# Optimization experiments

Hardware: AMD Instinct MI355X
Metric: run time of the kernel (lower is better)

The kernel has to match this reference:

```python
import jax, jax.numpy as jnp
import numpy as np

EPS_REG = 0.1     # Sinkhorn regularization eps (init arg)
MAX_ITER = 50     # max Sinkhorn iterations (init arg)
THRESH = 0.1      # early-stop threshold from the torch code

N, P1, P2, D = 4, 2048, 2048, 64


def setup_inputs() -> dict:
    key = jax.random.key(0)
    k1, k2, k3 = jax.random.split(key, 3)
    x = jax.random.normal(k1, (N, P1, D), dtype=jnp.float32)
    y = jax.random.normal(k2, (N, P2, D), dtype=jnp.float32)
    M = jax.random.normal(k3, (D, D), dtype=jnp.float32)
    return {"x": x, "y": y, "M": M}


def _cost_matrix(x, y, M):
    # C_ij = (x_i - y_j) M (x_i - y_j)^T, expanded to avoid the [N,P1,P2,D]
    # difference tensor the torch code materializes (identical math):
    #   C = x M x^T (diag) + y M y^T (diag) - x M y^T - (y M x^T)^T
    xM = jnp.einsum('npd,de->npe', x, M)
    yM = jnp.einsum('nqd,de->nqe', y, M)
    dx = jnp.einsum('npd,npd->np', xM, x)  # [N,P1]
    dy = jnp.einsum('nqd,nqd->nq', yM, y)  # [N,P2]
    cross = jnp.einsum('npd,nqd->npq', xM, y) + jnp.einsum('nqd,npd->npq', yM, x)
    return dx[:, :, None] + dy[:, None, :] - cross  # [N,P1,P2]


def _bias(C, u, v, eps):
    # M_ij = (-C_ij + u_i + v_j) / eps
    return (-C + u[..., :, None] + v[..., None, :]) / eps


def _sinkhorn(C, eps):
    n, p1, p2 = C.shape
    log_mu = jnp.log(jnp.full((n, p1), 1.0 / p1, C.dtype) + 1e-8)
    log_nu = jnp.log(jnp.full((n, p2), 1.0 / p2, C.dtype) + 1e-8)
    u0 = jnp.zeros((n, p1), C.dtype)
    v0 = jnp.zeros((n, p2), C.dtype)

    def step(carry, _):
        u, v, active = carry
        u1 = u
        u_new = eps * (log_mu - jax.scipy.special.logsumexp(_bias(C, u, v, eps), axis=-1)) + u
        u = jnp.where(active, u_new, u)
        v_new = eps * (log_nu - jax.scipy.special.logsumexp(_bias(C, u, v, eps), axis=-2)) + v
        v = jnp.where(active, v_new, v)
        err = jnp.mean(jnp.sum(jnp.abs(u - u1), axis=-1))
        active = active & (err >= THRESH)  # freeze updates once converged (== torch break)
        return (u, v, active), None

    (u, v, _), _ = jax.lax.scan(step, (u0, v0, jnp.asarray(True)), None, length=MAX_ITER)
    return u, v


def reference(x, y, M):
    eps = EPS_REG
    C = _cost_matrix(x, y, M)
    u, v = _sinkhorn(C, eps)
    pi = jnp.exp(_bias(C, u, v, eps))
    cost = jnp.sum(pi * C, axis=(-2, -1))  # reduction='none' -> shape [N]
    return cost, pi, C
```

## Files before the change

kernel.cpp:

```cpp
#include <hip/hip_runtime.h>
#include <cstdint>
#include <cstddef>

#define NB 4
#define P1 2048
#define P2 2048
#define DD 64
#define ITER 50
#define EPS 0.1f
#define INV_EPS 10.0f
#define THRESH 0.1f
#define LOG_MU -7.6245985f
#define ELOG (-0.76245985f)
#define MU_VAL 0.00048829125f
#define ERRSLOTS 32
#define RP (P2 / 4)
#define PCHUNKS 128

__global__ void prep0(const float* __restrict__ M, float* __restrict__ S,
                      float* __restrict__ errAcc, int* __restrict__ active,
                      float* __restrict__ cost) {
    int t = threadIdx.x;
    for (int k = t; k < DD * DD; k += 256) {
        int d = k >> 6, e = k & 63;
        S[k] = M[d * DD + e] + M[e * DD + d];
    }
    for (int k = t; k < ITER * ERRSLOTS; k += 256) errAcc[k] = 0.0f;
    if (t < 64) active[t] = (t == 0) ? 1 : 0;
    if (t < NB) cost[t] = 0.0f;
}

__global__ __launch_bounds__(256) void prep1(const float* __restrict__ x,
                                             const float* __restrict__ y,
                                             const float* __restrict__ S,
                                             float* __restrict__ xS,
                                             float* __restrict__ dx,
                                             float* __restrict__ dy,
                                             float* __restrict__ u,
                                             float* __restrict__ v) {
    __shared__ float Sl[DD * DD];
    int t = threadIdx.x;
    for (int k = t; k < DD * DD; k += 256) Sl[k] = S[k];
    __syncthreads();
    int wave = t >> 6, lane = t & 63;
    int r = blockIdx.x * 4 + wave;
    bool isX = r < NB * P1;
    const float* src = isX ? x : y;
    int rr = isX ? r : r - NB * P1;
    float xv = src[(size_t)rr * DD + lane];
    float acc = 0.0f;
    #pragma unroll
    for (int d = 0; d < DD; ++d) {
        float xd = __shfl(xv, d, 64);
        acc = fmaf(xd, Sl[d * DD + lane], acc);
    }
    float p = acc * xv;
    #pragma unroll
    for (int o = 32; o; o >>= 1) p += __shfl_xor(p, o, 64);
    if (isX) {
        xS[(size_t)rr * DD + lane] = acc;
        if (lane == 0) { dx[rr] = 0.5f * p; u[rr] = 0.0f; }
    } else {
        if (lane == 0) { dy[rr] = 0.5f * p; v[rr] = 0.0f; }
    }
}

__global__ __launch_bounds__(256) void gemmC(const float* __restrict__ xS,
                                             const float* __restrict__ y,
                                             const float* __restrict__ dx,
                                             const float* __restrict__ dy,
                                             float* __restrict__ C) {
    __shared__ float xs[64][68];
    __shared__ float ys[64][68];
    int n = blockIdx.z;
    int i0 = blockIdx.y * 64, j0 = blockIdx.x * 64;
    int t = threadIdx.x;

    #pragma unroll
    for (int k = 0; k < 4; ++k) {
        int f = t + 256 * k;
        int row = f >> 4;
        int c4 = f & 15;
        float4 a = ((const float4*)xS)[((size_t)(n * P1 + i0 + row)) * (DD / 4) + c4];
        xs[4 * c4 + 0][row] = a.x; xs[4 * c4 + 1][row] = a.y;
        xs[4 * c4 + 2][row] = a.z; xs[4 * c4 + 3][row] = a.w;
        float4 b = ((const float4*)y)[((size_t)(n * P2 + j0 + row)) * (DD / 4) + c4];
        ys[4 * c4 + 0][row] = b.x; ys[4 * c4 + 1][row] = b.y;
        ys[4 * c4 + 2][row] = b.z; ys[4 * c4 + 3][row] = b.w;
    }
    __syncthreads();

    int tx = t & 15, ty = t >> 4;
    float acc[4][4] = {};
    #pragma unroll
    for (int e = 0; e < 64; ++e) {
        float4 a = *(const float4*)&xs[e][4 * ty];
        float4 b = *(const float4*)&ys[e][4 * tx];
        acc[0][0] = fmaf(a.x, b.x, acc[0][0]); acc[0][1] = fmaf(a.x, b.y, acc[0][1]);
        acc[0][2] = fmaf(a.x, b.z, acc[0][2]); acc[0][3] = fmaf(a.x, b.w, acc[0][3]);
        acc[1][0] = fmaf(a.y, b.x, acc[1][0]); acc[1][1] = fmaf(a.y, b.y, acc[1][1]);
        acc[1][2] = fmaf(a.y, b.z, acc[1][2]); acc[1][3] = fmaf(a.y, b.w, acc[1][3]);
        acc[2][0] = fmaf(a.z, b.x, acc[2][0]); acc[2][1] = fmaf(a.z, b.y, acc[2][1]);
        acc[2][2] = fmaf(a.z, b.z, acc[2][2]); acc[2][3] = fmaf(a.z, b.w, acc[2][3]);
        acc[3][0] = fmaf(a.w, b.x, acc[3][0]); acc[3][1] = fmaf(a.w, b.y, acc[3][1]);
        acc[3][2] = fmaf(a.w, b.z, acc[3][2]); acc[3][3] = fmaf(a.w, b.w, acc[3][3]);
    }

    int iBase = i0 + ty * 4, jBase = j0 + tx * 4;
    float4 dy4 = *(const float4*)&dy[n * P2 + jBase];
    #pragma unroll
    for (int r = 0; r < 4; ++r) {
        float dxv = dx[n * P1 + iBase + r];
        float4 o;
        o.x = dxv + dy4.x - acc[r][0];
        o.y = dxv + dy4.y - acc[r][1];
        o.z = dxv + dy4.z - acc[r][2];
        o.w = dxv + dy4.w - acc[r][3];
        *(float4*)&C[((size_t)(n * P1 + iBase + r)) * P2 + jBase] = o;
    }
}

__device__ __forceinline__ void load_row8(float4 dst[8], const float4* base, int lane) {
    #pragma unroll
    for (int k = 0; k < 8; ++k) dst[k] = base[lane + 64 * k];
}

__device__ __forceinline__ float row_lse(float4 c[8], float ai, const float* bl, int lane) {
    float m = -3.4e38f;
    #pragma unroll
    for (int k = 0; k < 8; ++k) {
        float4 vv = ((const float4*)bl)[lane + 64 * k];
        c[k].x = (ai - c[k].x) + vv.x;
        c[k].y = (ai - c[k].y) + vv.y;
        c[k].z = (ai - c[k].z) + vv.z;
        c[k].w = (ai - c[k].w) + vv.w;
        m = fmaxf(m, fmaxf(fmaxf(c[k].x, c[k].y), fmaxf(c[k].z, c[k].w)));
    }
    #pragma unroll
    for (int o = 1; o < 64; o <<= 1) m = fmaxf(m, __shfl_xor(m, o, 64));
    float s = 0.0f;
    #pragma unroll
    for (int k = 0; k < 8; ++k)
        s += __expf((c[k].x - m) * INV_EPS) + __expf((c[k].y - m) * INV_EPS) +
             __expf((c[k].z - m) * INV_EPS) + __expf((c[k].w - m) * INV_EPS);
    #pragma unroll
    for (int o = 1; o < 64; o <<= 1) s += __shfl_xor(s, o, 64);
    return EPS * __logf(s) + m;
}

__device__ __forceinline__ void mergec(float& m, float& s, float q) {
    float nm = fmaxf(m, q);
    s = s * __expf((m - nm) * INV_EPS) + __expf((q - nm) * INV_EPS);
    m = nm;
}
__device__ __forceinline__ void mergems(float& m, float& s, float mo, float so) {
    float nm = fmaxf(m, mo);
    s = s * __expf((m - nm) * INV_EPS) + so * __expf((mo - nm) * INV_EPS);
    m = nm;
}
__device__ __forceinline__ void merge44(float4& m, float4& s, float4 mo, float4 so) {
    mergems(m.x, s.x, mo.x, so.x);
    mergems(m.y, s.y, mo.y, so.y);
    mergems(m.z, s.z, mo.z, so.z);
    mergems(m.w, s.w, mo.w, so.w);
}

__device__ __forceinline__ void merge_row(float4 M[8], float4 S[8],
                                          const float4 q[8], float dr) {
    #pragma unroll
    for (int k = 0; k < 8; ++k) {
        mergec(M[k].x, S[k].x, q[k].x + dr);
        mergec(M[k].y, S[k].y, q[k].y + dr);
        mergec(M[k].z, S[k].z, q[k].z + dr);
        mergec(M[k].w, S[k].w, q[k].w + dr);
    }
}

__global__ __launch_bounds__(256) void iter_pass(const float* __restrict__ C,
                                                 float* __restrict__ u,
                                                 const float* __restrict__ v,
                                                 float* __restrict__ pm,
                                                 float* __restrict__ ps,
                                                 float* __restrict__ errAcc,
                                                 const int* __restrict__ active,
                                                 int t_iter) {
    if (!active[t_iter]) return;
    __shared__ float bl[P2];
    __shared__ float4 LM[4][512];
    __shared__ float4 LS[4][512];
    __shared__ float da_s[4];
    int t = threadIdx.x;
    int n = blockIdx.x >> 7;
    int i0 = (blockIdx.x & (PCHUNKS - 1)) * 16;
    {
        const float4* bsrc = (const float4*)(v + n * P2);
        ((float4*)bl)[t] = bsrc[t];
        ((float4*)bl)[t + 256] = bsrc[t + 256];
    }
    __syncthreads();

    int wave = t >> 6, lane = t & 63;
    int irow = i0 + wave * 4;
    float* arow = u + n * P1 + irow;
    float a0 = arow[0], a1 = arow[1], a2 = arow[2], a3 = arow[3];
    const float4* base = (const float4*)(C + ((size_t)(n * P1 + irow)) * P2);

    float4 M[8], S[8];
    #pragma unroll
    for (int k = 0; k < 8; ++k) {
        M[k] = make_float4(-3.4e38f, -3.4e38f, -3.4e38f, -3.4e38f);
        S[k] = make_float4(0.0f, 0.0f, 0.0f, 0.0f);
    }

    float4 A[8], B[8];
    load_row8(A, base, lane);
    load_row8(B, base + RP, lane);
    float l0 = row_lse(A, a0, bl, lane);
    float d0 = ELOG - l0;
    merge_row(M, S, A, d0);
    load_row8(A, base + 2 * RP, lane);
    float l1 = row_lse(B, a1, bl, lane);
    float d1 = ELOG - l1;
    merge_row(M, S, B, d1);
    load_row8(B, base + 3 * RP, lane);
    float l2 = row_lse(A, a2, bl, lane);
    float d2 = ELOG - l2;
    merge_row(M, S, A, d2);
    float l3 = row_lse(B, a3, bl, lane);
    float d3 = ELOG - l3;
    merge_row(M, S, B, d3);

    if (lane == 0) {
        arow[0] = a0 + d0; arow[1] = a1 + d1;
        arow[2] = a2 + d2; arow[3] = a3 + d3;
        da_s[wave] = fabsf(d0) + fabsf(d1) + fabsf(d2) + fabsf(d3);
    }

    #pragma unroll
    for (int k = 0; k < 8; ++k) {
        LM[wave][lane + 64 * k] = M[k];
        LS[wave][lane + 64 * k] = S[k];
    }
    __syncthreads();

    float4* pm4 = (float4*)pm;
    float4* ps4 = (float4*)ps;
    size_t pb4 = (size_t)blockIdx.x * 512;
    #pragma unroll
    for (int sl = 0; sl < 2; ++sl) {
        int slot = t + 256 * sl;
        float4 m = LM[0][slot], s = LS[0][slot];
        merge44(m, s, LM[1][slot], LS[1][slot]);
        merge44(m, s, LM[2][slot], LS[2][slot]);
        merge44(m, s, LM[3][slot], LS[3][slot]);
        pm4[pb4 + slot] = m;
        ps4[pb4 + slot] = s;
    }

    if (t == 0) {
        atomicAdd(&errAcc[t_iter * ERRSLOTS + (blockIdx.x & (ERRSLOTS - 1))],
                  da_s[0] + da_s[1] + da_s[2] + da_s[3]);
    }
}

__global__ __launch_bounds__(256) void v_comb(const float* __restrict__ pm,
                                              const float* __restrict__ ps,
                                              float* __restrict__ v,
                                              const float* __restrict__ errAcc,
                                              int* __restrict__ active,
                                              int t_iter) {
    if (blockIdx.x == 0 && threadIdx.x == 0) {
        float e = 0.0f;
        #pragma unroll
        for (int q = 0; q < ERRSLOTS; ++q) e += errAcc[t_iter * ERRSLOTS + q];
        if (active[t_iter] && (e * 0.25f >= THRESH)) active[t_iter + 1] = 1;
    }
    if (!active[t_iter]) return;
    __shared__ float LMv[4][64];
    __shared__ float LSv[4][64];
    int t = threadIdx.x, wave = t >> 6, lane = t & 63;
    int n = blockIdx.x >> 5;
    int j = ((blockIdx.x & 31) << 6) + lane;
    const float* pmb = pm + ((size_t)(n * PCHUNKS + wave * 32)) * P2 + j;
    const float* psb = ps + ((size_t)(n * PCHUNKS + wave * 32)) * P2 + j;
    float m0 = -3.4e38f, s0 = 0.0f, m1 = -3.4e38f, s1 = 0.0f;
    float m2 = -3.4e38f, s2 = 0.0f, m3 = -3.4e38f, s3 = 0.0f;
    #pragma unroll
    for (int c = 0; c < 32; c += 4) {
        mergems(m0, s0, pmb[(size_t)(c + 0) * P2], psb[(size_t)(c + 0) * P2]);
        mergems(m1, s1, pmb[(size_t)(c + 1) * P2], psb[(size_t)(c + 1) * P2]);
        mergems(m2, s2, pmb[(size_t)(c + 2) * P2], psb[(size_t)(c + 2) * P2]);
        mergems(m3, s3, pmb[(size_t)(c + 3) * P2], psb[(size_t)(c + 3) * P2]);
    }
    mergems(m0, s0, m1, s1);
    mergems(m2, s2, m3, s3);
    mergems(m0, s0, m2, s2);
    LMv[wave][lane] = m0; LSv[wave][lane] = s0;
    __syncthreads();
    if (wave == 0) {
        float m = LMv[0][lane], s = LSv[0][lane];
        mergems(m, s, LMv[1][lane], LSv[1][lane]);
        mergems(m, s, LMv[2][lane], LSv[2][lane]);
        mergems(m, s, LMv[3][lane], LSv[3][lane]);
        float lse = EPS * __logf(s) + m;
        v[n * P2 + j] = v[n * P2 + j] + ELOG - lse;
    }
}

__device__ __forceinline__ float row_sum(float4 c[8], float aiv, const float* bl,
                                         int lane) {
    float s = 0.0f;
    #pragma unroll
    for (int k = 0; k < 8; ++k) {
        float4 vv = ((const float4*)bl)[lane + 64 * k];
        c[k].x = __expf(fmaf(c[k].x, -INV_EPS, aiv + vv.x));
        c[k].y = __expf(fmaf(c[k].y, -INV_EPS, aiv + vv.y));
        c[k].z = __expf(fmaf(c[k].z, -INV_EPS, aiv + vv.z));
        c[k].w = __expf(fmaf(c[k].w, -INV_EPS, aiv + vv.w));
        s += (c[k].x + c[k].y) + (c[k].z + c[k].w);
    }
    #pragma unroll
    for (int o = 1; o < 64; o <<= 1) s += __shfl_xor(s, o, 64);
    return s;
}

__device__ __forceinline__ void acc_row(float4 S[8], const float4 q[8], float ed) {
    #pragma unroll
    for (int k = 0; k < 8; ++k) {
        S[k].x = fmaf(q[k].x, ed, S[k].x);
        S[k].y = fmaf(q[k].y, ed, S[k].y);
        S[k].z = fmaf(q[k].z, ed, S[k].z);
        S[k].w = fmaf(q[k].w, ed, S[k].w);
    }
}

__global__ __launch_bounds__(256) void iter_fast(const float* __restrict__ C,
                                                 float* __restrict__ u,
                                                 const float* __restrict__ v,
                                                 float* __restrict__ ps,
                                                 float* __restrict__ errAcc,
                                                 const int* __restrict__ active,
                                                 int t_iter) {
    if (!active[t_iter]) return;
    __shared__ float bl[P2];
    __shared__ float4 LS[4][512];
    __shared__ float da_s[4];
    int t = threadIdx.x;
    int n = blockIdx.x >> 7;
    int i0 = (blockIdx.x & (PCHUNKS - 1)) * 16;
    {
        const float4* bsrc = (const float4*)(v + n * P2);
        float4 b0 = bsrc[t], b1 = bsrc[t + 256];
        b0.x *= INV_EPS; b0.y *= INV_EPS; b0.z *= INV_EPS; b0.w *= INV_EPS;
        b1.x *= INV_EPS; b1.y *= INV_EPS; b1.z *= INV_EPS; b1.w *= INV_EPS;
        ((float4*)bl)[t] = b0;
        ((float4*)bl)[t + 256] = b1;
    }
    __syncthreads();

    int wave = t >> 6, lane = t & 63;
    int irow = i0 + wave * 4;
    float* arow = u + n * P1 + irow;
    float a0 = arow[0], a1 = arow[1], a2 = arow[2], a3 = arow[3];
    const float4* base = (const float4*)(C + ((size_t)(n * P1 + irow)) * P2);

    float4 S[8];
    #pragma unroll
    for (int k = 0; k < 8; ++k) S[k] = make_float4(0.0f, 0.0f, 0.0f, 0.0f);

    float4 X[8], Y[8], Z[8];
    load_row8(X, base, lane);
    load_row8(Y, base + RP, lane);
    load_row8(Z, base + 2 * RP, lane);
    float s0 = row_sum(X, a0 * INV_EPS, bl, lane);
    float d0 = ELOG - EPS * __logf(s0);
    acc_row(S, X, __fdividef(MU_VAL, s0));
    load_row8(X, base + 3 * RP, lane);
    float s1 = row_sum(Y, a1 * INV_EPS, bl, lane);
    float d1 = ELOG - EPS * __logf(s1);
    acc_row(S, Y, __fdividef(MU_VAL, s1));
    float s2 = row_sum(Z, a2 * INV_EPS, bl, lane);
    float d2 = ELOG - EPS * __logf(s2);
    acc_row(S, Z, __fdividef(MU_VAL, s2));
    float s3 = row_sum(X, a3 * INV_EPS, bl, lane);
    float d3 = ELOG - EPS * __logf(s3);
    acc_row(S, X, __fdividef(MU_VAL, s3));

    if (lane == 0) {
        arow[0] = a0 + d0; arow[1] = a1 + d1;
        arow[2] = a2 + d2; arow[3] = a3 + d3;
        da_s[wave] = fabsf(d0) + fabsf(d1) + fabsf(d2) + fabsf(d3);
    }

    #pragma unroll
    for (int k = 0; k < 8; ++k) LS[wave][lane + 64 * k] = S[k];
    __syncthreads();

    float4* ps4 = (float4*)ps;
    size_t pb4 = (size_t)blockIdx.x * 512;
    #pragma unroll
    for (int sl = 0; sl < 2; ++sl) {
        int slot = t + 256 * sl;
        float4 x0 = LS[0][slot], x1 = LS[1][slot];
        float4 x2 = LS[2][slot], x3 = LS[3][slot];
        float4 o;
        o.x = (x0.x + x1.x) + (x2.x + x3.x);
        o.y = (x0.y + x1.y) + (x2.y + x3.y);
        o.z = (x0.z + x1.z) + (x2.z + x3.z);
        o.w = (x0.w + x1.w) + (x2.w + x3.w);
        ps4[pb4 + slot] = o;
    }

    if (t == 0) {
        atomicAdd(&errAcc[t_iter * ERRSLOTS + (blockIdx.x & (ERRSLOTS - 1))],
                  da_s[0] + da_s[1] + da_s[2] + da_s[3]);
    }
}

__global__ __launch_bounds__(256) void v_fast(const float* __restrict__ ps,
                                              float* __restrict__ v,
                                              const float* __restrict__ errAcc,
                                              int* __restrict__ active,
                                              int t_iter) {
    if (blockIdx.x == 0 && threadIdx.x == 0) {
        float e = 0.0f;
        #pragma unroll
        for (int q = 0; q < ERRSLOTS; ++q) e += errAcc[t_iter * ERRSLOTS + q];
        if (active[t_iter] && (e * 0.25f >= THRESH)) active[t_iter + 1] = 1;
    }
    if (!active[t_iter]) return;
    __shared__ float LSv[4][64];
    int t = threadIdx.x, wave = t >> 6, lane = t & 63;
    int n = blockIdx.x >> 5;
    int j = ((blockIdx.x & 31) << 6) + lane;
    const float* psb = ps + ((size_t)(n * PCHUNKS + wave * 32)) * P2 + j;
    float s0 = 0.0f, s1 = 0.0f, s2 = 0.0f, s3 = 0.0f;
    #pragma unroll
    for (int c = 0; c < 32; c += 4) {
        s0 += psb[(size_t)(c + 0) * P2];
        s1 += psb[(size_t)(c + 1) * P2];
        s2 += psb[(size_t)(c + 2) * P2];
        s3 += psb[(size_t)(c + 3) * P2];
    }
    LSv[wave][lane] = (s0 + s1) + (s2 + s3);
    __syncthreads();
    if (wave == 0) {
        float s = (LSv[0][lane] + LSv[1][lane]) + (LSv[2][lane] + LSv[3][lane]);
        v[n * P2 + j] = v[n * P2 + j] + ELOG - EPS * __logf(s);
    }
}

__device__ __forceinline__ float row_pi(const float4 c[8], float ui, const float* vl,
                                        int lane, float4* prow) {
    float acc = 0.0f;
    #pragma unroll
    for (int k = 0; k < 8; ++k) {
        float4 vv = ((const float4*)vl)[lane + 64 * k];
        float4 p;
        p.x = __expf(((ui - c[k].x) + vv.x) * INV_EPS);
        p.y = __expf(((ui - c[k].y) + vv.y) * INV_EPS);
        p.z = __expf(((ui - c[k].z) + vv.z) * INV_EPS);
        p.w = __expf(((ui - c[k].w) + vv.w) * INV_EPS);
        prow[lane + 64 * k] = p;
        acc += p.x * c[k].x + p.y * c[k].y + p.z * c[k].z + p.w * c[k].w;
    }
    return acc;
}

__global__ __launch_bounds__(256) void final_pass(const float* __restrict__ C,
                                                  const float* __restrict__ u,
                                                  const float* __restrict__ v,
                                                  float* __restrict__ pi,
                                                  float* __restrict__ cost) {
    __shared__ float vl[P2];
    __shared__ float red[4];
    int t = threadIdx.x;
    int n = blockIdx.x >> 7;
    int i0 = (blockIdx.x & 127) * 16;
    {
        const float4* vsrc = (const float4*)(v + n * P2);
        ((float4*)vl)[t] = vsrc[t];
        ((float4*)vl)[t + 256] = vsrc[t + 256];
    }
    __syncthreads();

    int wave = t >> 6, lane = t & 63;
    int irow = i0 + wave * 4;
    const float* urow = u + n * P1 + irow;
    float u0 = urow[0], u1 = urow[1], u2 = urow[2], u3 = urow[3];
    const float4* base = (const float4*)(C + ((size_t)(n * P1 + irow)) * P2);
    float4* pbase = (float4*)(pi + ((size_t)(n * P1 + irow)) * P2);

    float4 A[8], B[8];
    load_row8(A, base, lane);
    load_row8(B, base + RP, lane);
    float acc = row_pi(A, u0, vl, lane, pbase);
    load_row8(A, base + 2 * RP, lane);
    acc += row_pi(B, u1, vl, lane, pbase + RP);
    load_row8(B, base + 3 * RP, lane);
    acc += row_pi(A, u2, vl, lane, pbase + 2 * RP);
    acc += row_pi(B, u3, vl, lane, pbase + 3 * RP);

    #pragma unroll
    for (int o = 1; o < 64; o <<= 1) acc += __shfl_xor(acc, o, 64);
    if (lane == 0) red[wave] = acc;
    __syncthreads();
    if (t == 0) atomicAdd(&cost[n], red[0] + red[1] + red[2] + red[3]);
}

extern "C" void kernel_launch(void* const* d_in, const int* in_sizes, int n_in,
                              void* d_out, int out_size, void* d_ws, size_t ws_size,
                              hipStream_t stream) {
    const float* x = (const float*)d_in[0];
    const float* y = (const float*)d_in[1];
    const float* M = (const float*)d_in[2];
    float* out = (float*)d_out;
    float* cost = out;
    float* pi = out + NB;
    float* C = out + NB + (size_t)NB * P1 * P2;

    float* ws = (float*)d_ws;
    float* S      = ws;
    float* xS     = S + DD * DD;
    float* dx     = xS + (size_t)NB * P1 * DD;
    float* dy     = dx + NB * P1;
    float* u      = dy + NB * P2;
    float* v      = u + NB * P1;
    float* errAcc = v + NB * P2;
    int*   active = (int*)(errAcc + ITER * ERRSLOTS);
    float* ws_end = (float*)(active + 64);

    size_t base_floats = (size_t)(ws_end - ws);
    size_t pmps_floats = 2 * (size_t)NB * PCHUNKS * P2;
    float* pm;
    float* ps;
    if (ws_size >= (base_floats + pmps_floats) * sizeof(float)) {
        pm = ws_end;
        ps = ws_end + pmps_floats / 2;
    } else {
        pm = pi;
        ps = pi + pmps_floats / 2;
    }

    prep0<<<1, 256, 0, stream>>>(M, S, errAcc, active, cost);
    prep1<<<(NB * (P1 + P2)) / 4, 256, 0, stream>>>(x, y, S, xS, dx, dy, u, v);
    gemmC<<<dim3(P2 / 64, P1 / 64, NB), 256, 0, stream>>>(xS, y, dx, dy, C);
    iter_pass<<<NB * PCHUNKS, 256, 0, stream>>>(C, u, v, pm, ps, errAcc, active, 0);
    v_comb<<<NB * 32, 256, 0, stream>>>(pm, ps, v, errAcc, active, 0);
    for (int t = 1; t < ITER; ++t) {
        iter_fast<<<NB * PCHUNKS, 256, 0, stream>>>(C, u, v, ps, errAcc, active, t);
        v_fast<<<NB * 32, 256, 0, stream>>>(ps, v, errAcc, active, t);
    }
    final_pass<<<NB * P1 / 16, 256, 0, stream>>>(C, u, v, pi, cost);
}
```

Before: 1.100 ms.

## Fuse column update into row iteration using atomic column-sum buffers

Removes the separate v_fast kernel per Sinkhorn iteration. Each row block now atomically adds its partial column sums into a per-iteration zeroed buffer, and the next iteration's kernel rebuilds v from that buffer with ping-pong v buffers. The convergence check also moves into that next kernel, and a final v_fin kernel applies the last update. This halves the number of launches and drops the partial-sum write and reread traffic. In exchange it adds float atomics, which are nondeterministic in summation order, plus a larger zeroing pass.

After: 2.096 ms. 1.91x slower.

```diff
diff --git a/kernel.cpp b/kernel.cpp
--- a/kernel.cpp
+++ b/kernel.cpp
@@ -19,15 +19,17 @@
 
 __global__ void prep0(const float* __restrict__ M, float* __restrict__ S,
                       float* __restrict__ errAcc, int* __restrict__ active,
-                      float* __restrict__ cost) {
-    int t = threadIdx.x;
-    for (int k = t; k < DD * DD; k += 256) {
+                      float* __restrict__ cost, float* __restrict__ Zb) {
+    int tid = blockIdx.x * 256 + threadIdx.x;
+    int stride = gridDim.x * 256;
+    for (int k = tid; k < DD * DD; k += stride) {
         int d = k >> 6, e = k & 63;
         S[k] = M[d * DD + e] + M[e * DD + d];
     }
-    for (int k = t; k < ITER * ERRSLOTS; k += 256) errAcc[k] = 0.0f;
-    if (t < 64) active[t] = (t == 0) ? 1 : 0;
-    if (t < NB) cost[t] = 0.0f;
+    for (int k = tid; k < ITER * ERRSLOTS; k += stride) errAcc[k] = 0.0f;
+    for (int k = tid; k < ITER * NB * P2; k += stride) Zb[k] = 0.0f;
+    if (tid < 64) active[tid] = (tid == 0) ? 1 : 0;
+    if (tid < NB) cost[tid] = 0.0f;
 }
 
 __global__ __launch_bounds__(256) void prep1(const float* __restrict__ x,
@@ -334,13 +336,14 @@
     }
 }
 
-__global__ __launch_bounds__(256) void iter_fast(const float* __restrict__ C,
-                                                 float* __restrict__ u,
-                                                 const float* __restrict__ v,
-                                                 float* __restrict__ ps,
-                                                 float* __restrict__ errAcc,
-                                                 const int* __restrict__ active,
-                                                 int t_iter) {
+__global__ __launch_bounds__(256) void iter_fused(const float* __restrict__ C,
+                                                  float* __restrict__ u,
+                                                  float* __restrict__ vb0,
+                                                  float* __restrict__ vb1,
+                                                  float* __restrict__ Zb,
+                                                  float* __restrict__ errAcc,
+                                                  int* __restrict__ active,
+                                                  int t_iter) {
     if (!active[t_iter]) return;
     __shared__ float bl[P2];
     __shared__ float4 LS[4][512];
@@ -348,11 +351,44 @@
     int t = threadIdx.x;
     int n = blockIdx.x >> 7;
     int i0 = (blockIdx.x & (PCHUNKS - 1)) * 16;
+
+    if (blockIdx.x == 0 && t == 0) {
+        float e = 0.0f;
+        #pragma unroll
+        for (int q = 0; q < ERRSLOTS; ++q) e += errAcc[(t_iter - 1) * ERRSLOTS + q];
+        if (e * 0.25f >= THRESH) active[t_iter + 1] = 1;
+    }
+
     {
-        const float4* bsrc = (const float4*)(v + n * P2);
-        float4 b0 = bsrc[t], b1 = bsrc[t + 256];
-        b0.x *= INV_EPS; b0.y *= INV_EPS; b0.z *= INV_EPS; b0.w *= INV_EPS;
-        b1.x *= INV_EPS; b1.y *= INV_EPS; b1.z *= INV_EPS; b1.w *= INV_EPS;
+        float4 vn0, vn1;
+        if (t_iter == 1) {
+            const float4* v04 = (const float4*)(vb0 + n * P2);
+            vn0 = v04[t]; vn1 = v04[t + 256];
+        } else {
+            const float* vp = (t_iter & 1) ? vb1 : vb0;
+            float* vw = (t_iter & 1) ? vb0 : vb1;
+            const float4* vp4 = (const float4*)(vp + n * P2);
+            const float4* zp4 = (const float4*)(Zb + ((size_t)(t_iter - 1) * NB + n) * P2);
+            float4 a0 = vp4[t], a1 = vp4[t + 256];
+            float4 z0 = zp4[t], z1 = zp4[t + 256];
+            vn0.x = a0.x + (ELOG - EPS * __logf(z0.x));
+            vn0.y = a0.y + (ELOG - EPS * __logf(z0.y));
+            vn0.z = a0.z + (ELOG - EPS * __logf(z0.z));
+            vn0.w = a0.w + (ELOG - EPS * __logf(z0.w));
+            vn1.x = a1.x + (ELOG - EPS * __logf(z1.x));
+            vn1.y = a1.y + (ELOG - EPS * __logf(z1.y));
+            vn1.z = a1.z + (ELOG - EPS * __logf(z1.z));
+            vn1.w = a1.w + (ELOG - EPS * __logf(z1.w));
+            if ((blockIdx.x & (PCHUNKS - 1)) == 0) {
+                float4* vw4 = (float4*)(vw + n * P2);
+                vw4[t] = vn0; vw4[t + 256] = vn1;
+            }
+        }
+        float4 b0, b1;
+        b0.x = vn0.x * INV_EPS; b0.y = vn0.y * INV_EPS;
+        b0.z = vn0.z * INV_EPS; b0.w = vn0.w * INV_EPS;
+        b1.x = vn1.x * INV_EPS; b1.y = vn1.y * INV_EPS;
+        b1.z = vn1.z * INV_EPS; b1.w = vn1.w * INV_EPS;
         ((float4*)bl)[t] = b0;
         ((float4*)bl)[t + 256] = b1;
     }
@@ -368,10 +404,10 @@
     #pragma unroll
     for (int k = 0; k < 8; ++k) S[k] = make_float4(0.0f, 0.0f, 0.0f, 0.0f);
 
-    float4 X[8], Y[8], Z[8];
+    float4 X[8], Y[8], Zr[8];
     load_row8(X, base, lane);
     load_row8(Y, base + RP, lane);
-    load_row8(Z, base + 2 * RP, lane);
+    load_row8(Zr, base + 2 * RP, lane);
     float s0 = row_sum(X, a0 * INV_EPS, bl, lane);
     float d0 = ELOG - EPS * __logf(s0);
     acc_row(S, X, __fdividef(MU_VAL, s0));
@@ -379,9 +415,9 @@
     float s1 = row_sum(Y, a1 * INV_EPS, bl, lane);
     float d1 = ELOG - EPS * __logf(s1);
     acc_row(S, Y, __fdividef(MU_VAL, s1));
-    float s2 = row_sum(Z, a2 * INV_EPS, bl, lane);
+    float s2 = row_sum(Zr, a2 * INV_EPS, bl, lane);
     float d2 = ELOG - EPS * __logf(s2);
-    acc_row(S, Z, __fdividef(MU_VAL, s2));
+    acc_row(S, Zr, __fdividef(MU_VAL, s2));
     float s3 = row_sum(X, a3 * INV_EPS, bl, lane);
     float d3 = ELOG - EPS * __logf(s3);
     acc_row(S, X, __fdividef(MU_VAL, s3));
@@ -396,8 +432,7 @@
     for (int k = 0; k < 8; ++k) LS[wave][lane + 64 * k] = S[k];
     __syncthreads();
 
-    float4* ps4 = (float4*)ps;
-    size_t pb4 = (size_t)blockIdx.x * 512;
+    float* zt = Zb + ((size_t)t_iter * NB + n) * P2;
     #pragma unroll
     for (int sl = 0; sl < 2; ++sl) {
         int slot = t + 256 * sl;
@@ -408,7 +443,11 @@
         o.y = (x0.y + x1.y) + (x2.y + x3.y);
         o.z = (x0.z + x1.z) + (x2.z + x3.z);
         o.w = (x0.w + x1.w) + (x2.w + x3.w);
-        ps4[pb4 + slot] = o;
+        int j = 4 * slot;
+        atomicAdd(&zt[j + 0], o.x);
+        atomicAdd(&zt[j + 1], o.y);
+        atomicAdd(&zt[j + 2], o.z);
+        atomicAdd(&zt[j + 3], o.w);
     }
 
     if (t == 0) {
@@ -417,37 +456,16 @@
     }
 }
 
-__global__ __launch_bounds__(256) void v_fast(const float* __restrict__ ps,
-                                              float* __restrict__ v,
-                                              const float* __restrict__ errAcc,
-                                              int* __restrict__ active,
-                                              int t_iter) {
-    if (blockIdx.x == 0 && threadIdx.x == 0) {
-        float e = 0.0f;
-        #pragma unroll
-        for (int q = 0; q < ERRSLOTS; ++q) e += errAcc[t_iter * ERRSLOTS + q];
-        if (active[t_iter] && (e * 0.25f >= THRESH)) active[t_iter + 1] = 1;
-    }
-    if (!active[t_iter]) return;
-    __shared__ float LSv[4][64];
-    int t = threadIdx.x, wave = t >> 6, lane = t & 63;
-    int n = blockIdx.x >> 5;
-    int j = ((blockIdx.x & 31) << 6) + lane;
-    const float* psb = ps + ((size_t)(n * PCHUNKS + wave * 32)) * P2 + j;
-    float s0 = 0.0f, s1 = 0.0f, s2 = 0.0f, s3 = 0.0f;
-    #pragma unroll
-    for (int c = 0; c < 32; c += 4) {
-        s0 += psb[(size_t)(c + 0) * P2];
-        s1 += psb[(size_t)(c + 1) * P2];
-        s2 += psb[(size_t)(c + 2) * P2];
-        s3 += psb[(size_t)(c + 3) * P2];
-    }
-    LSv[wave][lane] = (s0 + s1) + (s2 + s3);
-    __syncthreads();
-    if (wave == 0) {
-        float s = (LSv[0][lane] + LSv[1][lane]) + (LSv[2][lane] + LSv[3][lane]);
-        v[n * P2 + j] = v[n * P2 + j] + ELOG - EPS * __logf(s);
-    }
+__global__ void v_fin(float* __restrict__ v, const float* __restrict__ v2,
+                      const float* __restrict__ Zb, const int* __restrict__ active) {
+    int k = 0;
+    for (int q = 1; q < ITER; ++q) if (active[q]) k = q;
+    if (k == 0) return;
+    int n = blockIdx.x >> 3;
+    int j = ((blockIdx.x & 7) << 8) + threadIdx.x;
+    const float* vb = ((k - 1) & 1) ? v2 : v;
+    float zv = Zb[((size_t)k * NB + n) * P2 + j];
+    v[n * P2 + j] = vb[n * P2 + j] + ELOG - EPS * __logf(zv);
 }
 
 __device__ __forceinline__ float row_pi(const float4 c[8], float ui, const float* vl,
@@ -528,28 +546,21 @@
     float* v      = u + NB * P1;
     float* errAcc = v + NB * P2;
     int*   active = (int*)(errAcc + ITER * ERRSLOTS);
-    float* ws_end = (float*)(active + 64);
-
-    size_t base_floats = (size_t)(ws_end - ws);
-    size_t pmps_floats = 2 * (size_t)NB * PCHUNKS * P2;
-    float* pm;
-    float* ps;
-    if (ws_size >= (base_floats + pmps_floats) * sizeof(float)) {
-        pm = ws_end;
-        ps = ws_end + pmps_floats / 2;
-    } else {
-        pm = pi;
-        ps = pi + pmps_floats / 2;
-    }
-
-    prep0<<<1, 256, 0, stream>>>(M, S, errAcc, active, cost);
+    float* v2     = (float*)(active + 64);
+
+    float* Zb = pi;
+    float* pm = Zb + (size_t)ITER * NB * P2;
+    float* ps = pm + (size_t)NB * PCHUNKS * P2;
+
+    prep0<<<128, 256, 0, stream>>>(M, S, errAcc, active, cost, Zb);
     prep1<<<(NB * (P1 + P2)) / 4, 256, 0, stream>>>(x, y, S, xS, dx, dy, u, v);
     gemmC<<<dim3(P2 / 64, P1 / 64, NB), 256, 0, stream>>>(xS, y, dx, dy, C);
     iter_pass<<<NB * PCHUNKS, 256, 0, stream>>>(C, u, v, pm, ps, errAcc, active, 0);
     v_comb<<<NB * 32, 256, 0, stream>>>(pm, ps, v, errAcc, active, 0);
     for (int t = 1; t < ITER; ++t) {
-        iter_fast<<<NB * PCHUNKS, 256, 0, stream>>>(C, u, v, ps, errAcc, active, t);
-        v_fast<<<NB * 32, 256, 0, stream>>>(ps, v, errAcc, active, t);
-    }
+        iter_fused<<<NB * PCHUNKS, 256, 0, stream>>>(C, u, v, v2, Zb, errAcc,
+                                                     active, t);
+    }
+    v_fin<<<32, 256, 0, stream>>>(v, v2, Zb, active);
     final_pass<<<NB * P1 / 16, 256, 0, stream>>>(C, u, v, pi, cost);
 }
```
